# Performance work log

Hardware: AMD Instinct MI355X
Metric: run time of the kernel (lower is better)

Reference implementation:

```python
import jax, jax.numpy as jnp
import numpy as np

NUM_HEADS = 16
QKV_FEATURES = 2048
HEAD_DIM = QKV_FEATURES // NUM_HEADS
THETA = 10000.0


def compute_freqs_cis(dim, length, start_pos=0, theta=THETA, dtype=jnp.float32):
    freqs = 1.0 / theta ** (jnp.arange(0, dim, 2, dtype=jnp.float32) / dim)
    t = jnp.arange(length, dtype=jnp.float32) + start_pos
    freqs = jnp.outer(t, freqs)  # (L, dim//2)
    return jnp.sin(freqs).astype(dtype), jnp.cos(freqs).astype(dtype)


def apply_rotary_emb(x, sin, cos):
    # x: (B, L, H, D); sin/cos: (L, D//2); interleaved-pair rotation
    x1 = x[..., 0::2]
    x2 = x[..., 1::2]
    sin = sin[None, :, None, :]
    cos = cos[None, :, None, :]
    y1 = x1 * cos - x2 * sin
    y2 = x1 * sin + x2 * cos
    return jnp.stack([y1, y2], axis=-1).reshape(x.shape)


def setup_inputs() -> dict:
    key = jax.random.key(0)
    ks = jax.random.split(key, 6)
    B, L, E = 2, 2048, 2048
    s_in = 1.0 / np.sqrt(E)
    s_out = 1.0 / np.sqrt(QKV_FEATURES)
    return {
        "x": jax.random.normal(ks[0], (B, L, E), jnp.float32),
        "Wq": jax.random.normal(ks[1], (E, QKV_FEATURES), jnp.float32) * s_in,
        "Wk": jax.random.normal(ks[2], (E, QKV_FEATURES), jnp.float32) * s_in,
        "Wv": jax.random.normal(ks[3], (E, QKV_FEATURES), jnp.float32) * s_in,
        "Wo": jax.random.normal(ks[4], (QKV_FEATURES, E), jnp.float32) * s_out,
        "bo": jnp.zeros((E,), jnp.float32),
    }


def reference(x, Wq, Wk, Wv, Wo, bo):
    B, L, E = x.shape
    H, D = NUM_HEADS, HEAD_DIM

    q = (x @ Wq).reshape(B, L, H, D)
    k = (x @ Wk).reshape(B, L, H, D)
    v = (x @ Wv).reshape(B, L, H, D)

    sin, cos = compute_freqs_cis(D, L)
    q = apply_rotary_emb(q, sin, cos)
    k = apply_rotary_emb(k, sin, cos)

    scale = D ** (-0.5)
    sim = jnp.einsum("bqhd,bkhd->bhqk", q, k) * scale

    pos = jnp.arange(L)
    causal_mask = pos[None, :] <= pos[:, None]  # (Lq, Lk)
    sim = jnp.where(causal_mask[None, None, :, :], sim, -1e9)

    attn = jax.nn.softmax(sim, axis=-1)
    out = jnp.einsum("bhqk,bkhd->bqhd", attn, v).reshape(B, L, H * D)
    return out @ Wo + bo
```

## Files before the change

### kernel.cpp

```cpp
#include <hip/hip_runtime.h>
#include <hip/hip_bf16.h>
#include <stdint.h>
#include <stddef.h>

#define B_   2
#define L_   2048
#define E_   2048
#define H_   16
#define D_   128
#define F_   2048
#define NROW (B_*L_)
#define QS   6144

typedef __bf16 bf16_t;
typedef __bf16 bf16x4 __attribute__((ext_vector_type(4)));
typedef __bf16 bf16x8 __attribute__((ext_vector_type(8)));
typedef float  f32x4  __attribute__((ext_vector_type(4)));

__device__ __forceinline__ void gload16(const void* g, void* l) {
  __builtin_amdgcn_global_load_lds(
      (const __attribute__((address_space(1))) void*)g,
      (__attribute__((address_space(3))) void*)l, 16, 0, 0);
}

#define VMC(n)  asm volatile("s_waitcnt vmcnt(" #n ")" ::: "memory")
#define BAR_MID do { asm volatile("" ::: "memory"); __builtin_amdgcn_s_barrier(); \
  asm volatile("s_waitcnt lgkmcnt(0)" ::: "memory"); __builtin_amdgcn_sched_barrier(0); } while(0)
#define BAR_END do { asm volatile("" ::: "memory"); __builtin_amdgcn_s_barrier(); } while(0)

__global__ __launch_bounds__(256) void k_prep(const float* __restrict__ x,
                                              const float* __restrict__ Wq,
                                              const float* __restrict__ Wk,
                                              const float* __restrict__ Wv,
                                              const float* __restrict__ Wo,
                                              bf16_t* __restrict__ xb,
                                              bf16_t* __restrict__ wqkvt,
                                              bf16_t* __restrict__ wot,
                                              float2* __restrict__ sc) {
  const int bb = blockIdx.x;
  if (bb < 8192) {
    int i = bb*256 + threadIdx.x;
    float4 v = ((const float4*)x)[i];
    bf16x4 t;
    t[0] = (__bf16)v.x; t[1] = (__bf16)v.y; t[2] = (__bf16)v.z; t[3] = (__bf16)v.w;
    ((bf16x4*)xb)[i] = t;
  } else if (bb < 24576) {
    __shared__ float tile[32][33];
    const int r4 = bb - 8192;
    const int z  = r4 >> 12;
    const int xy = r4 & 4095;
    const int ct = xy & 63, rt = xy >> 6;
    const float* in = (z == 0) ? Wq : (z == 1) ? Wk : (z == 2) ? Wv : Wo;
    bf16_t* out = (z < 3) ? wqkvt + (size_t)z*F_*E_ : wot;
    const int c = threadIdx.x & 31, r0 = threadIdx.x >> 5;
    #pragma unroll
    for (int k = 0; k < 4; k++) {
      int r = r0 + k*8;
      tile[r][c] = in[(size_t)(rt*32 + r)*2048 + ct*32 + c];
    }
    __syncthreads();
    #pragma unroll
    for (int k = 0; k < 4; k++) {
      int r = r0 + k*8;
      out[(size_t)(ct*32 + r)*2048 + rt*32 + c] = (__bf16)tile[c][r];
    }
  } else {
    int id = (bb - 24576)*256 + threadIdx.x;
    int t = id >> 6, i = id & 63;
    float freq = powf(10000.0f, -(float)i / 64.0f);
    float a = (float)t * freq;
    sc[id] = make_float2(cosf(a), sinf(a));
  }
}

__global__ __launch_bounds__(256) void k_vt(const bf16_t* __restrict__ qkv,
                                            bf16_t* __restrict__ vt) {
  __shared__ bf16_t tile[32][33];
  const int bb = blockIdx.x;
  const int lt = bb & 63, dt = (bb >> 6) & 3, bh = bb >> 8;
  const int b = bh >> 4, h = bh & 15;
  const int c = threadIdx.x & 31, r0 = threadIdx.x >> 5;
  #pragma unroll
  for (int k = 0; k < 4; k++) {
    int r = r0 + k*8;
    tile[r][c] = qkv[(size_t)(b*L_ + lt*32 + r)*QS + 2*F_ + h*D_ + dt*32 + c];
  }
  __syncthreads();
  #pragma unroll
  for (int k = 0; k < 4; k++) {
    int r = r0 + k*8;
    vt[(size_t)(bh*D_ + dt*32 + r)*L_ + lt*32 + c] = tile[c][r];
  }
}

#define RDA(BASE) do { _Pragma("unroll") for (int m_=0;m_<4;m_++) { \
  a[m_][0] = *(const bf16x8*)((BASE) + m_*2048 + cs0); \
  a[m_][1] = *(const bf16x8*)((BASE) + m_*2048 + cs1); } } while(0)
#define RDB(BASE, NB) do { _Pragma("unroll") for (int n_=0;n_<2;n_++) { \
  bb_[n_][0] = *(const bf16x8*)((BASE) + ((NB)+n_)*2048 + cs0); \
  bb_[n_][1] = *(const bf16x8*)((BASE) + ((NB)+n_)*2048 + cs1); } } while(0)
#define MMQ(NB) do { __builtin_amdgcn_s_setprio(1); \
  _Pragma("unroll") for (int m_=0;m_<4;m_++) { \
    _Pragma("unroll") for (int n_=0;n_<2;n_++) { \
      acc[m_][(NB)+n_] = __builtin_amdgcn_mfma_f32_16x16x32_bf16(a[m_][0], bb_[n_][0], acc[m_][(NB)+n_], 0, 0, 0); \
      acc[m_][(NB)+n_] = __builtin_amdgcn_mfma_f32_16x16x32_bf16(a[m_][1], bb_[n_][1], acc[m_][(NB)+n_], 0, 0, 0); } } \
  __builtin_amdgcn_s_setprio(0); } while(0)

template<typename OutT, int MODE>
__global__ __launch_bounds__(512, 1) void k_gemm256(const bf16_t* __restrict__ A,
                                                    const bf16_t* __restrict__ BT,
                                                    OutT* __restrict__ C,
                                                    const float* __restrict__ bias,
                                                    const float2* __restrict__ sc,
                                                    float qscale,
                                                    int M, int N, int K) {
  __shared__ char sm[147456];
  const int tid = threadIdx.x, lane = tid & 63, wave = tid >> 6;
  const int wr = wave >> 2, wc = wave & 3;
  const int lr = lane & 15, lg = lane >> 4;
  const int nbx = N >> 8;
  const int band = nbx >> 3;
  const int bid = blockIdx.x;
  const int idx = bid >> 3;
  const int bx = (bid & 7)*band + idx % band;
  const int by = idx / band;
  const int row0 = by << 7, col0 = bx << 8;
  const int sr  = tid >> 3;
  const int sxe = ((tid & 7) ^ (sr & 7)) << 3;
  const bf16_t* Ag = A  + (size_t)(row0 + sr)*K + sxe;
  const bf16_t* Bg = BT + (size_t)(col0 + sr)*K + sxe;
  auto stA = [&](int t) {
    const bf16_t* s = Ag + t*64;
    char* d = sm + (t % 3)*16384 + wave*1024;
    gload16(s, d); gload16(s + (size_t)64*K, d + 8192);
  };
  auto stB01 = [&](int t) {
    const bf16_t* s = Bg + t*64;
    char* d = sm + 49152 + (t % 3)*32768 + wave*1024;
    gload16(s, d); gload16(s + (size_t)64*K, d + 8192);
  };
  auto stB23 = [&](int t) {
    const bf16_t* s = Bg + (size_t)128*K + t*64;
    char* d = sm + 49152 + (t % 3)*32768 + 16384 + wave*1024;
    gload16(s, d); gload16(s + (size_t)64*K, d + 8192);
  };
  const int cs0 = (lg ^ (lr & 7)) << 4;
  const int cs1 = ((4 + lg) ^ (lr & 7)) << 4;

  f32x4 acc[4][4] = {};
  bf16x8 a[4][2], bb_[2][2];

  stA(0); stB01(0); stB23(0);
  stA(1); stB01(1); stB23(1);
  VMC(6);
  BAR_END;

  const int nt = K >> 6;
  for (int u = 0; u < nt; u++) {
    const int bi = u % 3;
    const char* Ab = sm + bi*16384 + (wr*64 + lr)*128;
    const char* Bb = sm + 49152 + bi*32768 + (wc*64 + lr)*128;
    RDA(Ab);
    RDB(Bb, 0);
    if (u + 2 < nt) { stA(u+2); stB01(u+2); }
    BAR_MID;
    MMQ(0);
    BAR_END;
    RDB(Bb, 2);
    if (u + 2 < nt) stB23(u+2);
    BAR_MID;
    MMQ(2);
    if (u + 2 < nt) { VMC(6); } else { VMC(0); }
    BAR_END;
  }
  #pragma unroll
  for (int m = 0; m < 4; m++) {
    #pragma unroll
    for (int n = 0; n < 4; n++) {
      const int col = col0 + wc*64 + n*16 + lr;
      if (MODE == 2) {
        const float bv = bias[col];
        #pragma unroll
        for (int j = 0; j < 4; j++) {
          const int row = row0 + wr*64 + m*16 + lg*4 + j;
          C[(size_t)row*N + col] = (OutT)(acc[m][n][j] + bv);
        }
      } else {
        const int third = col >> 11;
        const int ii    = (col & (D_-1)) >> 1;
        const bool odd  = (lr & 1);
        const float ss  = (third == 0) ? qscale : 1.0f;
        #pragma unroll
        for (int j = 0; j < 4; j++) {
          const int row = row0 + wr*64 + m*16 + lg*4 + j;
          const float v0 = acc[m][n][j];
          const float vp = __shfl_xor(v0, 1);
          float res;
          if (third == 2) {
            res = v0;
          } else {
            const int t = row & (L_-1);
            const float2 cs = sc[t*64 + ii];
            const float cosv = cs.x * ss, sinv = cs.y * ss;
            res = odd ? (vp*sinv + v0*cosv) : (v0*cosv - vp*sinv);
          }
          C[(size_t)row*N + col] = (OutT)res;
        }
      }
    }
  }
}

template<bool MASK>
__device__ __forceinline__ void attn_tile(
    int kv0, int wq0, int lr, int lg,
    const char* __restrict__ Kb, const char* __restrict__ Vb, char* __restrict__ Pb,
    const bf16x8 (&aq)[4], f32x4 (&o)[8], float& mrow, float& lsum) {
  const int swz = (lr & 7) << 4;
  f32x4 s[4] = {};
  #pragma unroll
  for (int kd = 0; kd < 4; kd++) {
    bf16x8 ak[4];
    #pragma unroll
    for (int n = 0; n < 4; n++)
      ak[n] = *(const bf16x8*)(Kb + (n*16 + lr)*256 + (((kd*4 + lg) << 4) ^ swz));
    __builtin_amdgcn_s_setprio(1);
    #pragma unroll
    for (int n = 0; n < 4; n++)
      s[n] = __builtin_amdgcn_mfma_f32_16x16x32_bf16(ak[n], aq[kd], s[n], 0, 0, 0);
    __builtin_amdgcn_s_setprio(0);
  }
  if (MASK) {
    const int q = wq0 + lr;
    #pragma unroll
    for (int n = 0; n < 4; n++)
      #pragma unroll
      for (int j = 0; j < 4; j++)
        if (kv0 + n*16 + lg*4 + j > q) s[n][j] = -30000.0f;
  }
  float pmax = fmaxf(
      fmaxf(fmaxf(fmaxf(s[0][0], s[0][1]), fmaxf(s[0][2], s[0][3])),
            fmaxf(fmaxf(s[1][0], s[1][1]), fmaxf(s[1][2], s[1][3]))),
      fmaxf(fmaxf(fmaxf(s[2][0], s[2][1]), fmaxf(s[2][2], s[2][3])),
            fmaxf(fmaxf(s[3][0], s[3][1]), fmaxf(s[3][2], s[3][3]))));
  pmax = fmaxf(pmax, __shfl_xor(pmax, 16));
  pmax = fmaxf(pmax, __shfl_xor(pmax, 32));
  if (!__all(pmax - mrow <= 8.0f)) {
    const float mnew = fmaxf(mrow, pmax);
    const float corr = exp2f(mrow - mnew);
    mrow = mnew;
    lsum *= corr;
    #pragma unroll
    for (int n2 = 0; n2 < 8; n2++) o[n2] *= corr;
  }
  float rs = 0.0f;
  #pragma unroll
  for (int n = 0; n < 4; n++)
    #pragma unroll
    for (int j = 0; j < 4; j++) {
      float p = exp2f(s[n][j] - mrow);
      s[n][j] = p;
      rs += p;
    }
  rs += __shfl_xor(rs, 16);
  rs += __shfl_xor(rs, 32);
  lsum += rs;
  #pragma unroll
  for (int n = 0; n < 4; n++) {
    bf16x4 pw;
    pw[0] = (__bf16)s[n][0]; pw[1] = (__bf16)s[n][1];
    pw[2] = (__bf16)s[n][2]; pw[3] = (__bf16)s[n][3];
    *(bf16x4*)(Pb + ((lr*128 + n*32 + lg*8) ^ swz)) = pw;
  }
  #pragma unroll
  for (int ks = 0; ks < 2; ks++) {
    bf16x8 pb = *(const bf16x8*)(Pb + ((lr*128 + ks*64 + lg*16) ^ swz));
    __builtin_amdgcn_s_setprio(1);
    #pragma unroll
    for (int n2 = 0; n2 < 8; n2++) {
      bf16x8 av = *(const bf16x8*)(Vb + (n2*16 + lr)*128 + (((ks*4 + lg) << 4) ^ swz));
      o[n2] = __builtin_amdgcn_mfma_f32_16x16x32_bf16(av, pb, o[n2], 0, 0, 0);
    }
    __builtin_amdgcn_s_setprio(0);
  }
}

__global__ __launch_bounds__(512, 4) void k_attn(const bf16_t* __restrict__ QKV,
                                                 const bf16_t* __restrict__ Vt,
                                                 bf16_t* __restrict__ O) {
  __shared__ bf16_t Ks[2][64*128];
  __shared__ bf16_t Vs[2][128*64];
  __shared__ bf16_t Pl[8][16*64];
  const int tid = threadIdx.x, lane = tid & 63, wave = tid >> 6;
  const int bidx = blockIdx.x;
  const int xcd = bidx & 7, idx = bidx >> 3;
  const int bh  = xcd*4 + (idx & 3);
  const int qt  = 15 - (idx >> 2);
  const int b = bh >> 4, h = bh & 15;
  const int wq0 = qt*128 + wave*16;
  const int lr = lane & 15, lg = lane >> 4;
  char* Pb = (char*)&Pl[wave][0];
  const bf16_t* Q = QKV;
  const bf16_t* K = QKV + F_;

  bf16x8 aq[4];
  #pragma unroll
  for (int kd = 0; kd < 4; kd++)
    aq[kd] = *(const bf16x8*)&Q[(size_t)(b*L_ + wq0 + lr)*QS + h*D_ + kd*32 + lg*8];

  const int kr = tid >> 4, kc = tid & 15;
  const bf16_t* Kg0 = K + (size_t)(b*L_ + kr)*QS + h*D_ + ((kc ^ (kr & 7)) << 3);
  const int vr = tid >> 3, vc = tid & 7;
  const bf16_t* Vg0 = Vt + (size_t)((b*H_ + h)*D_ + vr)*L_ + ((vc ^ (vr & 7)) << 3);

  f32x4 o[8] = {};
  float mrow = -3.0e38f, lsum = 0.0f;
  const int ntb   = 2*qt + 2;
  const int nfull = (wq0 + 1) >> 6;
  const int nmine = ((wq0 + 15) >> 6) + 1;

  {
    char* kb = (char*)&Ks[0][0] + wave*1024;
    char* vb = (char*)&Vs[0][0] + wave*1024;
    gload16(Kg0,                 kb);
    gload16(Kg0 + (size_t)32*QS, kb + 8192);
    gload16(Vg0,                 vb);
    gload16(Vg0 + (size_t)64*L_, vb + 8192);
  }
  __syncthreads();

  int buf = 0;
  for (int t = 0; t < ntb; t++) {
    if (t + 1 < ntb) {
      const int kn = (t+1)*64;
      char* kb = (char*)&Ks[buf^1][0] + wave*1024;
      char* vb = (char*)&Vs[buf^1][0] + wave*1024;
      const bf16_t* kg = Kg0 + (size_t)kn*QS;
      const bf16_t* vg = Vg0 + kn;
      gload16(kg,                 kb);
      gload16(kg + (size_t)32*QS, kb + 8192);
      gload16(vg,                 vb);
      gload16(vg + (size_t)64*L_, vb + 8192);
    }
    const char* Kb = (const char*)&Ks[buf][0];
    const char* Vb = (const char*)&Vs[buf][0];
    if (t < nfull)
      attn_tile<false>(t*64, wq0, lr, lg, Kb, Vb, Pb, aq, o, mrow, lsum);
    else if (t < nmine)
      attn_tile<true >(t*64, wq0, lr, lg, Kb, Vb, Pb, aq, o, mrow, lsum);
    __syncthreads();
    buf ^= 1;
  }
  const float inv = 1.0f / lsum;
  bf16_t* orow = O + (size_t)(b*L_ + wq0 + lr)*F_ + h*D_ + lg*4;
  #pragma unroll
  for (int n2 = 0; n2 < 8; n2++) {
    bf16x4 ov;
    ov[0] = (__bf16)(o[n2][0]*inv); ov[1] = (__bf16)(o[n2][1]*inv);
    ov[2] = (__bf16)(o[n2][2]*inv); ov[3] = (__bf16)(o[n2][3]*inv);
    *(bf16x4*)(orow + n2*16) = ov;
  }
}

extern "C" void kernel_launch(void* const* d_in, const int* in_sizes, int n_in,
                              void* d_out, int out_size, void* d_ws, size_t ws_size,
                              hipStream_t stream) {
  const float* x  = (const float*)d_in[0];
  const float* Wq = (const float*)d_in[1];
  const float* Wk = (const float*)d_in[2];
  const float* Wv = (const float*)d_in[3];
  const float* Wo = (const float*)d_in[4];
  const float* bo = (const float*)d_in[5];
  float* out = (float*)d_out;

  char* ws = (char*)d_ws;
  size_t off = 0;
  auto alloc = [&](size_t bytes) {
    char* p = ws + off;
    off = (off + bytes + 255) & ~(size_t)255;
    return p;
  };
  bf16_t* xb    = (bf16_t*)alloc((size_t)NROW*E_*2);
  bf16_t* wqkvt = (bf16_t*)alloc((size_t)3*F_*E_*2);
  bf16_t* wot   = (bf16_t*)alloc((size_t)F_*E_*2);
  float2* sc    = (float2*)alloc((size_t)L_*64*sizeof(float2));
  bf16_t* qkv   = (bf16_t*)alloc((size_t)NROW*QS*2);
  bf16_t* vt    = (bf16_t*)alloc((size_t)NROW*F_*2);
  bf16_t* ob    = xb;

  const float scale2 = 0.08838834764831845f * 1.44269504088896f;

  k_prep<<<dim3(25088), 256, 0, stream>>>(x, Wq, Wk, Wv, Wo, xb, wqkvt, wot, sc);

  k_gemm256<bf16_t, 1><<<dim3((QS/256)*(NROW/128)), 512, 0, stream>>>(
      xb, wqkvt, qkv, nullptr, sc, scale2, NROW, QS, E_);

  k_vt<<<dim3(8192), 256, 0, stream>>>(qkv, vt);

  k_attn<<<dim3(512), 512, 0, stream>>>(qkv, vt, ob);

  k_gemm256<float, 2><<<dim3((E_/256)*(NROW/128)), 512, 0, stream>>>(
      ob, wot, out, bo, nullptr, 1.0f, NROW, E_, F_);
}
```

Baseline: 423.2 us.

## Enlarge GEMM tiles to 256x256 with double buffering; shrink attention blocks to 64 rows

The GEMM kernel moves from 128x256 to 256x256 output tiles. Each wave now computes a 128x64 sub-tile with 8x4 accumulators, and the triple-buffered staging becomes a double-buffered schedule that interleaves the A/B half-tile loads across four MFMA phases. This raises arithmetic intensity per LDS byte and halves the grid size, at the cost of more accumulator registers and fewer blocks to spread across CUs. Attention blocks drop from 512 threads and 128 query rows to 256 threads and 64 query rows, doubling the grid to improve load balance across causal tiles.

```diff
diff --git a/kernel.cpp b/kernel.cpp
--- a/kernel.cpp
+++ b/kernel.cpp
@@ -93,17 +93,23 @@
   }
 }
 
-#define RDA(BASE) do { _Pragma("unroll") for (int m_=0;m_<4;m_++) { \
+#define RDA03(BASE) do { _Pragma("unroll") for (int m_=0;m_<4;m_++) { \
   a[m_][0] = *(const bf16x8*)((BASE) + m_*2048 + cs0); \
   a[m_][1] = *(const bf16x8*)((BASE) + m_*2048 + cs1); } } while(0)
-#define RDB(BASE, NB) do { _Pragma("unroll") for (int n_=0;n_<2;n_++) { \
-  bb_[n_][0] = *(const bf16x8*)((BASE) + ((NB)+n_)*2048 + cs0); \
-  bb_[n_][1] = *(const bf16x8*)((BASE) + ((NB)+n_)*2048 + cs1); } } while(0)
-#define MMQ(NB) do { __builtin_amdgcn_s_setprio(1); \
+#define RDA47(BASE) do { _Pragma("unroll") for (int m_=0;m_<4;m_++) { \
+  a[m_][0] = *(const bf16x8*)((BASE) + (m_+4)*2048 + cs0); \
+  a[m_][1] = *(const bf16x8*)((BASE) + (m_+4)*2048 + cs1); } } while(0)
+#define RDB01(BASE) do { _Pragma("unroll") for (int n_=0;n_<2;n_++) { \
+  b[n_][0] = *(const bf16x8*)((BASE) + n_*2048 + cs0); \
+  b[n_][1] = *(const bf16x8*)((BASE) + n_*2048 + cs1); } } while(0)
+#define RDB23(BASE) do { _Pragma("unroll") for (int n_=0;n_<2;n_++) { \
+  b[2+n_][0] = *(const bf16x8*)((BASE) + (2+n_)*2048 + cs0); \
+  b[2+n_][1] = *(const bf16x8*)((BASE) + (2+n_)*2048 + cs1); } } while(0)
+#define MM16(MB, NB) do { __builtin_amdgcn_s_setprio(1); \
   _Pragma("unroll") for (int m_=0;m_<4;m_++) { \
     _Pragma("unroll") for (int n_=0;n_<2;n_++) { \
-      acc[m_][(NB)+n_] = __builtin_amdgcn_mfma_f32_16x16x32_bf16(a[m_][0], bb_[n_][0], acc[m_][(NB)+n_], 0, 0, 0); \
-      acc[m_][(NB)+n_] = __builtin_amdgcn_mfma_f32_16x16x32_bf16(a[m_][1], bb_[n_][1], acc[m_][(NB)+n_], 0, 0, 0); } } \
+      acc[(MB)+m_][(NB)+n_] = __builtin_amdgcn_mfma_f32_16x16x32_bf16(a[m_][0], b[(NB)+n_][0], acc[(MB)+m_][(NB)+n_], 0, 0, 0); \
+      acc[(MB)+m_][(NB)+n_] = __builtin_amdgcn_mfma_f32_16x16x32_bf16(a[m_][1], b[(NB)+n_][1], acc[(MB)+m_][(NB)+n_], 0, 0, 0); } } \
   __builtin_amdgcn_s_setprio(0); } while(0)
 
 template<typename OutT, int MODE>
@@ -114,7 +120,7 @@
                                                     const float2* __restrict__ sc,
                                                     float qscale,
                                                     int M, int N, int K) {
-  __shared__ char sm[147456];
+  __shared__ char sm[131072];
   const int tid = threadIdx.x, lane = tid & 63, wave = tid >> 6;
   const int wr = wave >> 2, wc = wave & 3;
   const int lr = lane & 15, lg = lane >> 4;
@@ -124,57 +130,57 @@
   const int idx = bid >> 3;
   const int bx = (bid & 7)*band + idx % band;
   const int by = idx / band;
-  const int row0 = by << 7, col0 = bx << 8;
+  const int row0 = by << 8, col0 = bx << 8;
   const int sr  = tid >> 3;
   const int sxe = ((tid & 7) ^ (sr & 7)) << 3;
   const bf16_t* Ag = A  + (size_t)(row0 + sr)*K + sxe;
   const bf16_t* Bg = BT + (size_t)(col0 + sr)*K + sxe;
-  auto stA = [&](int t) {
-    const bf16_t* s = Ag + t*64;
-    char* d = sm + (t % 3)*16384 + wave*1024;
+  char* smA = sm;
+  char* smB = sm + 65536;
+  const int dst0 = wave*1024;
+  auto stA = [&](int buf, int h, int kt) {
+    const bf16_t* s = Ag + (size_t)(h*128)*K + kt;
+    char* d = smA + buf*32768 + h*16384 + dst0;
     gload16(s, d); gload16(s + (size_t)64*K, d + 8192);
   };
-  auto stB01 = [&](int t) {
-    const bf16_t* s = Bg + t*64;
-    char* d = sm + 49152 + (t % 3)*32768 + wave*1024;
-    gload16(s, d); gload16(s + (size_t)64*K, d + 8192);
-  };
-  auto stB23 = [&](int t) {
-    const bf16_t* s = Bg + (size_t)128*K + t*64;
-    char* d = sm + 49152 + (t % 3)*32768 + 16384 + wave*1024;
+  auto stB = [&](int buf, int h, int kt) {
+    const bf16_t* s = Bg + (size_t)(h*128)*K + kt;
+    char* d = smB + buf*32768 + h*16384 + dst0;
     gload16(s, d); gload16(s + (size_t)64*K, d + 8192);
   };
   const int cs0 = (lg ^ (lr & 7)) << 4;
   const int cs1 = ((4 + lg) ^ (lr & 7)) << 4;
 
-  f32x4 acc[4][4] = {};
-  bf16x8 a[4][2], bb_[2][2];
-
-  stA(0); stB01(0); stB23(0);
-  stA(1); stB01(1); stB23(1);
+  f32x4 acc[8][4] = {};
+  bf16x8 a[4][2], b[4][2];
+
+  stA(0,0,0); stA(0,1,0); stB(0,0,0); stB(0,1,0);
+  stA(1,0,64); stB(1,0,64); stB(1,1,64);
   VMC(6);
   BAR_END;
 
   const int nt = K >> 6;
   for (int u = 0; u < nt; u++) {
-    const int bi = u % 3;
-    const char* Ab = sm + bi*16384 + (wr*64 + lr)*128;
-    const char* Bb = sm + 49152 + bi*32768 + (wc*64 + lr)*128;
-    RDA(Ab);
-    RDB(Bb, 0);
-    if (u + 2 < nt) { stA(u+2); stB01(u+2); }
-    BAR_MID;
-    MMQ(0);
-    BAR_END;
-    RDB(Bb, 2);
-    if (u + 2 < nt) stB23(u+2);
-    BAR_MID;
-    MMQ(2);
-    if (u + 2 < nt) { VMC(6); } else { VMC(0); }
-    BAR_END;
-  }
-  #pragma unroll
-  for (int m = 0; m < 4; m++) {
+    const int buf = u & 1;
+    const char* Ab = smA + buf*32768 + wr*16384 + lr*128;
+    const char* Bb = smB + buf*32768 + (wc >> 1)*16384 + ((wc & 1)*64 + lr)*128;
+    RDA03(Ab); RDB01(Bb);
+    if (u + 1 < nt) stA(buf^1, 1, (u+1) << 6);
+    BAR_MID; MM16(0,0); BAR_END;
+    RDB23(Bb);
+    BAR_MID; MM16(0,2); BAR_END;
+    RDA47(Ab);
+    if (u + 2 < nt) { stB(buf, 0, (u+2) << 6); stB(buf, 1, (u+2) << 6); }
+    BAR_MID; MM16(4,0); BAR_END;
+    if (u + 2 < nt) {
+      stA(buf, 0, (u+2) << 6);
+      BAR_MID; MM16(4,2); VMC(6); BAR_END;
+    } else {
+      BAR_MID; MM16(4,2); VMC(0); BAR_END;
+    }
+  }
+  #pragma unroll
+  for (int m = 0; m < 8; m++) {
     #pragma unroll
     for (int n = 0; n < 4; n++) {
       const int col = col0 + wc*64 + n*16 + lr;
@@ -182,7 +188,7 @@
         const float bv = bias[col];
         #pragma unroll
         for (int j = 0; j < 4; j++) {
-          const int row = row0 + wr*64 + m*16 + lg*4 + j;
+          const int row = row0 + wr*128 + m*16 + lg*4 + j;
           C[(size_t)row*N + col] = (OutT)(acc[m][n][j] + bv);
         }
       } else {
@@ -192,7 +198,7 @@
         const float ss  = (third == 0) ? qscale : 1.0f;
         #pragma unroll
         for (int j = 0; j < 4; j++) {
-          const int row = row0 + wr*64 + m*16 + lg*4 + j;
+          const int row = row0 + wr*128 + m*16 + lg*4 + j;
           const float v0 = acc[m][n][j];
           const float vp = __shfl_xor(v0, 1);
           float res;
@@ -285,19 +291,19 @@
   }
 }
 
-__global__ __launch_bounds__(512, 4) void k_attn(const bf16_t* __restrict__ QKV,
+__global__ __launch_bounds__(256, 2) void k_attn(const bf16_t* __restrict__ QKV,
                                                  const bf16_t* __restrict__ Vt,
                                                  bf16_t* __restrict__ O) {
   __shared__ bf16_t Ks[2][64*128];
   __shared__ bf16_t Vs[2][128*64];
-  __shared__ bf16_t Pl[8][16*64];
+  __shared__ bf16_t Pl[4][16*64];
   const int tid = threadIdx.x, lane = tid & 63, wave = tid >> 6;
   const int bidx = blockIdx.x;
   const int xcd = bidx & 7, idx = bidx >> 3;
   const int bh  = xcd*4 + (idx & 3);
-  const int qt  = 15 - (idx >> 2);
+  const int qt  = 31 - (idx >> 2);
   const int b = bh >> 4, h = bh & 15;
-  const int wq0 = qt*128 + wave*16;
+  const int wq0 = qt*64 + wave*16;
   const int lr = lane & 15, lg = lane >> 4;
   char* Pb = (char*)&Pl[wave][0];
   const bf16_t* Q = QKV;
@@ -312,36 +318,31 @@
   const bf16_t* Kg0 = K + (size_t)(b*L_ + kr)*QS + h*D_ + ((kc ^ (kr & 7)) << 3);
   const int vr = tid >> 3, vc = tid & 7;
   const bf16_t* Vg0 = Vt + (size_t)((b*H_ + h)*D_ + vr)*L_ + ((vc ^ (vr & 7)) << 3);
+  const int dst0 = wave*1024;
+  auto stageKV = [&](int bufi, int kv) {
+    char* kb = (char*)&Ks[bufi][0] + dst0;
+    char* vb = (char*)&Vs[bufi][0] + dst0;
+    const bf16_t* kg = Kg0 + (size_t)kv*QS;
+    const bf16_t* vg = Vg0 + kv;
+    #pragma unroll
+    for (int i = 0; i < 4; i++) {
+      gload16(kg + (size_t)(i*16)*QS, kb + i*4096);
+      gload16(vg + (size_t)(i*32)*L_, vb + i*4096);
+    }
+  };
 
   f32x4 o[8] = {};
   float mrow = -3.0e38f, lsum = 0.0f;
-  const int ntb   = 2*qt + 2;
+  const int ntb   = qt + 1;
   const int nfull = (wq0 + 1) >> 6;
   const int nmine = ((wq0 + 15) >> 6) + 1;
 
-  {
-    char* kb = (char*)&Ks[0][0] + wave*1024;
-    char* vb = (char*)&Vs[0][0] + wave*1024;
-    gload16(Kg0,                 kb);
-    gload16(Kg0 + (size_t)32*QS, kb + 8192);
-    gload16(Vg0,                 vb);
-    gload16(Vg0 + (size_t)64*L_, vb + 8192);
-  }
+  stageKV(0, 0);
   __syncthreads();
 
   int buf = 0;
   for (int t = 0; t < ntb; t++) {
-    if (t + 1 < ntb) {
-      const int kn = (t+1)*64;
-      char* kb = (char*)&Ks[buf^1][0] + wave*1024;
-      char* vb = (char*)&Vs[buf^1][0] + wave*1024;
-      const bf16_t* kg = Kg0 + (size_t)kn*QS;
-      const bf16_t* vg = Vg0 + kn;
-      gload16(kg,                 kb);
-      gload16(kg + (size_t)32*QS, kb + 8192);
-      gload16(vg,                 vb);
-      gload16(vg + (size_t)64*L_, vb + 8192);
-    }
+    if (t + 1 < ntb) stageKV(buf^1, (t+1)*64);
     const char* Kb = (const char*)&Ks[buf][0];
     const char* Vb = (const char*)&Vs[buf][0];
     if (t < nfull)
@@ -392,13 +393,13 @@
 
   k_prep<<<dim3(25088), 256, 0, stream>>>(x, Wq, Wk, Wv, Wo, xb, wqkvt, wot, sc);
 
-  k_gemm256<bf16_t, 1><<<dim3((QS/256)*(NROW/128)), 512, 0, stream>>>(
+  k_gemm256<bf16_t, 1><<<dim3((QS/256)*(NROW/256)), 512, 0, stream>>>(
       xb, wqkvt, qkv, nullptr, sc, scale2, NROW, QS, E_);
 
   k_vt<<<dim3(8192), 256, 0, stream>>>(qkv, vt);
 
-  k_attn<<<dim3(512), 512, 0, stream>>>(qkv, vt, ob);
-
-  k_gemm256<float, 2><<<dim3((E_/256)*(NROW/128)), 512, 0, stream>>>(
+  k_attn<<<dim3(1024), 256, 0, stream>>>(qkv, vt, ob);
+
+  k_gemm256<float, 2><<<dim3((E_/256)*(NROW/256)), 512, 0, stream>>>(
       ob, wot, out, bo, nullptr, 1.0f, NROW, E_, F_);
 }
```

Result: slower. 449.6 us (+6.2%).
